# Kernel tuning notes

Hardware: AMD Instinct MI355X
Metric: run time of the kernel (lower is better)

Reference implementation:

```python
import jax, jax.numpy as jnp
import numpy as np

B = 1 << 20          # pixels (1024x1024 render)
RES = 512            # neural texture resolution
C_OFF = 8            # offset texture channels
C_RGB = 8            # rgb texture channels
HID = 32             # MLP hidden width
SLOPE = 0.01         # LeakyReLU negative slope (torch default)


def _leaky(x):
    return jnp.where(x >= 0, x, SLOPE * x)


def _mlp(x, params):
    # 3 hidden LeakyReLU layers + linear output, matching ThreeLayerMLP
    n = len(params)
    for i, (W, b) in enumerate(params):
        x = x @ W.T + b
        if i < n - 1:
            x = _leaky(x)
    return x


def _bilinear_wrap(tex, uv):
    # tex: (R, R, C) stored y-major; uv: (B, 2) in [0,1], wrapped (tiling texture)
    R = tex.shape[0]
    p = uv * R - 0.5
    i0 = jnp.floor(p).astype(jnp.int32)
    f = p - i0
    x0 = jnp.mod(i0[:, 0], R); x1 = jnp.mod(i0[:, 0] + 1, R)
    y0 = jnp.mod(i0[:, 1], R); y1 = jnp.mod(i0[:, 1] + 1, R)
    fx = f[:, 0:1]; fy = f[:, 1:2]
    v00 = tex[y0, x0]; v01 = tex[y0, x1]
    v10 = tex[y1, x0]; v11 = tex[y1, x1]
    return (v00 * (1 - fx) * (1 - fy) + v01 * fx * (1 - fy)
            + v10 * (1 - fx) * fy + v11 * fx * fy)


def _linear_params(key, n_in, n_out):
    W = jax.random.normal(key, (n_out, n_in), dtype=jnp.float32) * 0.01
    b = jnp.zeros((n_out,), dtype=jnp.float32)
    return W, b


def setup_inputs() -> dict:
    key = jax.random.key(0)
    ks = jax.random.split(key, 16)
    # directions: xy components of unit vectors, keep |xy| < 1
    camera_dir = (jax.random.uniform(ks[0], (B, 2), jnp.float32) - 0.5) * 1.2
    light_dir = (jax.random.uniform(ks[1], (B, 2), jnp.float32) - 0.5) * 1.2
    uv = jax.random.uniform(ks[2], (B, 2), jnp.float32)
    offset_tex = jax.random.normal(ks[3], (RES, RES, C_OFF), jnp.float32) * 0.1
    rgb_tex = jax.random.normal(ks[4], (RES, RES, C_RGB), jnp.float32) * 0.1
    # offset network: 10 -> 32 -> 32 -> 32 -> 1
    ow0, ob0 = _linear_params(ks[5], C_OFF + 2, HID)
    ow1, ob1 = _linear_params(ks[6], HID, HID)
    ow2, ob2 = _linear_params(ks[7], HID, HID)
    ow3, ob3 = _linear_params(ks[8], HID, 1)
    # rgb network: 12 -> 32 -> 32 -> 32 -> 3
    rw0, rb0 = _linear_params(ks[9], C_RGB + 4, HID)
    rw1, rb1 = _linear_params(ks[10], HID, HID)
    rw2, rb2 = _linear_params(ks[11], HID, HID)
    rw3, rb3 = _linear_params(ks[12], HID, 3)
    return dict(camera_dir=camera_dir, light_dir=light_dir, uv=uv,
                offset_tex=offset_tex, rgb_tex=rgb_tex,
                ow0=ow0, ob0=ob0, ow1=ow1, ob1=ob1, ow2=ow2, ob2=ob2, ow3=ow3, ob3=ob3,
                rw0=rw0, rb0=rb0, rw1=rw1, rb1=rb1, rw2=rw2, rb2=rb2, rw3=rw3, rb3=rb3)


def reference(camera_dir, light_dir, uv, offset_tex, rgb_tex,
              ow0, ob0, ow1, ob1, ow2, ob2, ow3, ob3,
              rw0, rb0, rw1, rb1, rw2, rb2, rw3, rb3):
    off_params = [(ow0, ob0), (ow1, ob1), (ow2, ob2), (ow3, ob3)]
    rgb_params = [(rw0, rb0), (rw1, rb1), (rw2, rb2), (rw3, rb3)]
    # offset branch: sample offset texture at uv, run tiny MLP -> neural depth
    off_lat = _bilinear_wrap(offset_tex, uv)                         # (B, 8)
    depth = _mlp(jnp.concatenate([off_lat, camera_dir], -1), off_params)  # (B, 1)
    # calculate_neural_offset: offset_uv = dir_xy / dir_z * depth
    z = jnp.sqrt(jnp.clip(1.0 - jnp.sum(camera_dir ** 2, -1, keepdims=True), 1e-6))
    uv2 = uv + camera_dir / z * depth                                # (B, 2)
    # rgb branch: sample rgb texture at offset intersection
    rgb_lat = _bilinear_wrap(rgb_tex, uv2)                           # (B, 8)
    rgb_in = jnp.concatenate([light_dir, camera_dir, rgb_lat], -1)   # (B, 12)
    return _mlp(rgb_in, rgb_params)                                  # (B, 3)
```

## Files before the change

kernel.cpp:

```cpp
#include <hip/hip_runtime.h>
#include <hip/hip_bf16.h>

static constexpr int BATCH = 1 << 20;
static constexpr size_t ILV_BYTES = (size_t)512 * 512 * 16 * 4;
static constexpr size_t WBLOB_BYTES = 768 * 16;

using f32x16 = __attribute__((ext_vector_type(16))) float;
using s16x8  = __attribute__((ext_vector_type(8))) short;
using u32x4  = __attribute__((ext_vector_type(4))) unsigned int;

__device__ __forceinline__ unsigned pkbf(float lo, float hi) {
  unsigned short a = __builtin_bit_cast(unsigned short, __float2bfloat16(lo));
  unsigned short b = __builtin_bit_cast(unsigned short, __float2bfloat16(hi));
  return (unsigned)a | ((unsigned)b << 16);
}

__device__ __forceinline__ u32x4 pack8(const float* __restrict__ p) {
  u32x4 r = {pkbf(p[0], p[1]), pkbf(p[2], p[3]), pkbf(p[4], p[5]), pkbf(p[6], p[7])};
  return r;
}

__device__ __forceinline__ f32x16 mfma_bf16(u32x4 a, u32x4 b, f32x16 c) {
  return __builtin_amdgcn_mfma_f32_32x32x16_bf16(
      __builtin_bit_cast(s16x8, a), __builtin_bit_cast(s16x8, b), c, 0, 0, 0);
}

__device__ __forceinline__ void act_pack_swap(f32x16 acc, u32x4& B0, u32x4& B1) {
  float r[16];
#pragma unroll
  for (int i = 0; i < 16; ++i) {
    float t = acc[i];
    r[i] = fmaxf(t, 0.01f * t);
  }
  unsigned pk[4][2];
#pragma unroll
  for (int b = 0; b < 4; ++b) {
    pk[b][0] = pkbf(r[4 * b + 0], r[4 * b + 1]);
    pk[b][1] = pkbf(r[4 * b + 2], r[4 * b + 3]);
  }
  auto r0 = __builtin_amdgcn_permlane32_swap(pk[0][0], pk[1][0], false, false);
  auto r1 = __builtin_amdgcn_permlane32_swap(pk[0][1], pk[1][1], false, false);
  auto r2 = __builtin_amdgcn_permlane32_swap(pk[2][0], pk[3][0], false, false);
  auto r3 = __builtin_amdgcn_permlane32_swap(pk[2][1], pk[3][1], false, false);
  B0[0] = r0[0]; B0[1] = r1[0]; B0[2] = r0[1]; B0[3] = r1[1];
  B1[0] = r2[0]; B1[1] = r3[0]; B1[2] = r2[1]; B1[3] = r3[1];
}

__device__ __forceinline__ f32x16 load_bias(const float* __restrict__ bp, int h) {
  f32x16 c;
#pragma unroll
  for (int b = 0; b < 4; ++b) {
    float4 t = *reinterpret_cast<const float4*>(bp + 8 * b + 4 * h);
    c[4 * b + 0] = t.x; c[4 * b + 1] = t.y; c[4 * b + 2] = t.z; c[4 * b + 3] = t.w;
  }
  return c;
}

template <bool ILV>
__device__ __forceinline__ float4 bilin4(const float* __restrict__ tex, float ux,
                                         float uy, int h, int which) {
  float px = ux * 512.0f - 0.5f;
  float py = uy * 512.0f - 0.5f;
  float fpx = floorf(px), fpy = floorf(py);
  float fx = px - fpx, fy = py - fpy;
  int ix = (int)fpx, iy = (int)fpy;
  int x0 = ix & 511, x1 = (ix + 1) & 511;
  int y0 = iy & 511, y1 = (iy + 1) & 511;
  constexpr int SH = ILV ? 4 : 3;
  const int co = (ILV ? (which << 3) : 0) + (h << 2);
  const float* p00 = tex + (((size_t)((y0 << 9) | x0) << SH) + co);
  const float* p01 = tex + (((size_t)((y0 << 9) | x1) << SH) + co);
  const float* p10 = tex + (((size_t)((y1 << 9) | x0) << SH) + co);
  const float* p11 = tex + (((size_t)((y1 << 9) | x1) << SH) + co);
  float4 a = *reinterpret_cast<const float4*>(p00);
  float4 b = *reinterpret_cast<const float4*>(p01);
  float4 c = *reinterpret_cast<const float4*>(p10);
  float4 d = *reinterpret_cast<const float4*>(p11);
  float gx = 1.0f - fx, gy = 1.0f - fy;
  float w00 = gx * gy, w01 = fx * gy, w10 = gx * fy, w11 = fx * fy;
  float4 o;
  o.x = fmaf(d.x, w11, fmaf(c.x, w10, fmaf(b.x, w01, a.x * w00)));
  o.y = fmaf(d.y, w11, fmaf(c.y, w10, fmaf(b.y, w01, a.y * w00)));
  o.z = fmaf(d.z, w11, fmaf(c.z, w10, fmaf(b.z, w01, a.z * w00)));
  o.w = fmaf(d.w, w11, fmaf(c.w, w10, fmaf(b.w, w01, a.w * w00)));
  return o;
}

__global__ void __launch_bounds__(256) tex_interleave(
    const float* __restrict__ t0, const float* __restrict__ t1,
    float* __restrict__ ws) {
  int i = blockIdx.x * 256 + threadIdx.x;
  int texel = i >> 2;
  int q = i & 3;
  const float* src = (q < 2 ? t0 : t1) + (((size_t)texel << 3) + ((q & 1) << 2));
  reinterpret_cast<float4*>(ws)[i] = *reinterpret_cast<const float4*>(src);
}

__global__ void __launch_bounds__(256) pack_weights(
    const float* __restrict__ ow0, const float* __restrict__ ow1,
    const float* __restrict__ ow2, const float* __restrict__ rw0,
    const float* __restrict__ rw1, const float* __restrict__ rw2,
    const float* __restrict__ rw3, u32x4* __restrict__ Wb) {
  int slot = blockIdx.x * 256 + threadIdx.x;
  if (slot < 768) {
    int F = slot % 12;
    int lb = slot / 12;
    int h = lb >> 5, m = lb & 31;
    u32x4 v = {0u, 0u, 0u, 0u};
    switch (F) {
      case 0:
        if (h == 0) v = pack8(ow0 + 10 * m);
        else { const float* p = ow0 + 10 * m + 8; v = u32x4{pkbf(p[0], p[1]), 0u, 0u, 0u}; }
        break;
      case 1: v = pack8(ow1 + 32 * m + 8 * h); break;
      case 2: v = pack8(ow1 + 32 * m + 16 + 8 * h); break;
      case 3: v = pack8(ow2 + 32 * m + 8 * h); break;
      case 4: v = pack8(ow2 + 32 * m + 16 + 8 * h); break;
      case 5:
        if (h == 0) v = pack8(rw0 + 12 * m);
        else { const float* p = rw0 + 12 * m + 8; v = u32x4{pkbf(p[0], p[1]), pkbf(p[2], p[3]), 0u, 0u}; }
        break;
      case 6: v = pack8(rw1 + 32 * m + 8 * h); break;
      case 7: v = pack8(rw1 + 32 * m + 16 + 8 * h); break;
      case 8: v = pack8(rw2 + 32 * m + 8 * h); break;
      case 9: v = pack8(rw2 + 32 * m + 16 + 8 * h); break;
      case 10: if (m < 3) v = pack8(rw3 + 32 * m + 8 * h); break;
      case 11: if (m < 3) v = pack8(rw3 + 32 * m + 16 + 8 * h); break;
    }
    Wb[slot] = v;
  }
}

template <bool ILV>
__global__ void __launch_bounds__(256) neumip_mfma(
    const float* __restrict__ cam_g, const float* __restrict__ light_g,
    const float* __restrict__ uv_g, const float* __restrict__ offset_tex,
    const float* __restrict__ rgb_tex, const float* __restrict__ wtex,
    const u32x4* __restrict__ Wb,
    const float* __restrict__ ow0, const float* __restrict__ ob0,
    const float* __restrict__ ow1, const float* __restrict__ ob1,
    const float* __restrict__ ow2, const float* __restrict__ ob2,
    const float* __restrict__ ow3, const float* __restrict__ ob3,
    const float* __restrict__ rw0, const float* __restrict__ rb0,
    const float* __restrict__ rw1, const float* __restrict__ rb1,
    const float* __restrict__ rw2, const float* __restrict__ rb2,
    const float* __restrict__ rw3, const float* __restrict__ rb3,
    float* __restrict__ out) {
  const int tid = threadIdx.x;
  const int lane = tid & 63;
  const int widx = tid >> 6;
  const int h = lane >> 5;
  const int sl = lane & 31;
  const int m = sl;
  const float* texO = ILV ? wtex : offset_tex;
  const float* texR = ILV ? wtex : rgb_tex;

  const int s1 = lane / 3, c1 = lane - 3 * s1;
  const int j2 = 64 + sl;
  const int s2 = j2 / 3, c2 = j2 - 3 * s2;

  const u32x4* Wl = Wb + (h * 32 + m) * 12;
  u32x4 A_o1, A_o2a, A_o2b, A_o3a, A_o3b, A_r1, A_r2a, A_r2b, A_r3a, A_r3b,
      A_r4a, A_r4b;
  if (ILV) {
    A_o1 = Wl[0];  A_o2a = Wl[1]; A_o2b = Wl[2]; A_o3a = Wl[3]; A_o3b = Wl[4];
    A_r1 = Wl[5];  A_r2a = Wl[6]; A_r2b = Wl[7]; A_r3a = Wl[8]; A_r3b = Wl[9];
    A_r4a = Wl[10]; A_r4b = Wl[11];
  } else {
    if (h == 0) {
      A_o1 = pack8(ow0 + 10 * m);
    } else {
      const float* p = ow0 + 10 * m + 8;
      A_o1 = u32x4{pkbf(p[0], p[1]), 0u, 0u, 0u};
    }
    A_o2a = pack8(ow1 + 32 * m + 8 * h);
    A_o2b = pack8(ow1 + 32 * m + 16 + 8 * h);
    A_o3a = pack8(ow2 + 32 * m + 8 * h);
    A_o3b = pack8(ow2 + 32 * m + 16 + 8 * h);
    if (h == 0) {
      A_r1 = pack8(rw0 + 12 * m);
    } else {
      const float* p = rw0 + 12 * m + 8;
      A_r1 = u32x4{pkbf(p[0], p[1]), pkbf(p[2], p[3]), 0u, 0u};
    }
    A_r2a = pack8(rw1 + 32 * m + 8 * h);
    A_r2b = pack8(rw1 + 32 * m + 16 + 8 * h);
    A_r3a = pack8(rw2 + 32 * m + 8 * h);
    A_r3b = pack8(rw2 + 32 * m + 16 + 8 * h);
    if (m < 3) {
      A_r4a = pack8(rw3 + 32 * m + 8 * h);
      A_r4b = pack8(rw3 + 32 * m + 16 + 8 * h);
    } else {
      A_r4a = u32x4{0u, 0u, 0u, 0u};
      A_r4b = u32x4{0u, 0u, 0u, 0u};
    }
  }

  f32x16 w3f;
#pragma unroll
  for (int b = 0; b < 4; ++b) {
    float4 t = *reinterpret_cast<const float4*>(ow3 + 8 * b + 4 * h);
    w3f[4 * b + 0] = t.x; w3f[4 * b + 1] = t.y;
    w3f[4 * b + 2] = t.z; w3f[4 * b + 3] = t.w;
  }
  const float b30 = rb3[0], b31 = rb3[1], b32 = rb3[2];
  const float ob3s = ob3[0];

  const float2* uv2g = reinterpret_cast<const float2*>(uv_g);
  const float2* cam2g = reinterpret_cast<const float2*>(cam_g);
  const float2* light2g = reinterpret_cast<const float2*>(light_g);

  const int NG = BATCH / 32;
  const int nw = (int)(gridDim.x * (blockDim.x >> 6));
  int g = (int)blockIdx.x * (int)(blockDim.x >> 6) + widx;
  if (g >= NG) return;

  float2 uvv = uv2g[g * 32 + sl];
  float2 cam = cam2g[g * 32 + sl];
  float2 light = light2g[g * 32 + sl];
  float4 ch = bilin4<ILV>(texO, uvv.x, uvv.y, h, 0);

#pragma unroll 1
  for (; g < NG; g += nw) {
    const int gn = (g + nw < NG) ? g + nw : g;
    const int Sn = gn * 32 + sl;
    float2 uvn = uv2g[Sn];
    float2 camn = cam2g[Sn];
    float2 lightn = light2g[Sn];

    unsigned V0 = pkbf(ch.x, ch.y), V1 = pkbf(ch.z, ch.w);
    auto t0 = __builtin_amdgcn_permlane32_swap(V0, V0, false, false);
    auto t1 = __builtin_amdgcn_permlane32_swap(V1, V1, false, false);
    unsigned camk = pkbf(cam.x, cam.y);
    u32x4 Bin;
    Bin[0] = h ? camk : V0;
    Bin[1] = h ? 0u : V1;
    Bin[2] = h ? 0u : t0[1];
    Bin[3] = h ? 0u : t1[1];

    f32x16 acc = load_bias(ob0, h);
    acc = mfma_bf16(A_o1, Bin, acc);
    u32x4 B0, B1;
    act_pack_swap(acc, B0, B1);
    acc = load_bias(ob1, h);
    acc = mfma_bf16(A_o2a, B0, acc);
    acc = mfma_bf16(A_o2b, B1, acc);
    act_pack_swap(acc, B0, B1);
    acc = load_bias(ob2, h);
    acc = mfma_bf16(A_o3a, B0, acc);
    acc = mfma_bf16(A_o3b, B1, acc);

    float part = 0.0f;
#pragma unroll
    for (int i = 0; i < 16; ++i) {
      float t = acc[i];
      t = fmaxf(t, 0.01f * t);
      part = fmaf(w3f[i], t, part);
    }
    float depth = part + __shfl_xor(part, 32) + ob3s;

    float s2f = fmaf(cam.x, cam.x, cam.y * cam.y);
    float z = sqrtf(fmaxf(1.0f - s2f, 1e-6f));
    float drz = depth * (1.0f / z);
    float u2x = fmaf(cam.x, drz, uvv.x);
    float u2y = fmaf(cam.y, drz, uvv.y);

    float4 chr = bilin4<ILV>(texR, u2x, u2y, h, 1);
    float4 chn = bilin4<ILV>(texO, uvn.x, uvn.y, h, 0);

    unsigned P0 = pkbf(chr.x, chr.y), P1 = pkbf(chr.z, chr.w);
    u32x4 Brin;
    Brin[0] = h ? P0 : pkbf(light.x, light.y);
    Brin[1] = h ? P1 : camk;
    Brin[2] = h ? 0u : P0;
    Brin[3] = h ? 0u : P1;

    acc = load_bias(rb0, h);
    acc = mfma_bf16(A_r1, Brin, acc);
    act_pack_swap(acc, B0, B1);
    acc = load_bias(rb1, h);
    acc = mfma_bf16(A_r2a, B0, acc);
    acc = mfma_bf16(A_r2b, B1, acc);
    act_pack_swap(acc, B0, B1);
    acc = load_bias(rb2, h);
    acc = mfma_bf16(A_r3a, B0, acc);
    acc = mfma_bf16(A_r3b, B1, acc);
    act_pack_swap(acc, B0, B1);
    f32x16 accf;
#pragma unroll
    for (int i = 0; i < 16; ++i) accf[i] = 0.0f;
    accf = mfma_bf16(A_r4a, B0, accf);
    accf = mfma_bf16(A_r4b, B1, accf);

    float o0 = accf[0] + b30, o1 = accf[1] + b31, o2 = accf[2] + b32;
    float a0 = __shfl(o0, s1), a1 = __shfl(o1, s1), a2 = __shfl(o2, s1);
    float v1 = (c1 == 0) ? a0 : ((c1 == 1) ? a1 : a2);
    float d0 = __shfl(o0, s2), d1 = __shfl(o1, s2), d2 = __shfl(o2, s2);
    float v2 = (c2 == 0) ? d0 : ((c2 == 1) ? d1 : d2);
    float* og = out + (size_t)g * 96;
    og[lane] = v1;
    if (h == 1) og[64 + sl] = v2;

    uvv = uvn; cam = camn; light = lightn; ch = chn;
  }
}

extern "C" void kernel_launch(void* const* d_in, const int* in_sizes, int n_in,
                              void* d_out, int out_size, void* d_ws, size_t ws_size,
                              hipStream_t stream) {
  const float* cam = (const float*)d_in[0];
  const float* light = (const float*)d_in[1];
  const float* uv = (const float*)d_in[2];
  const float* offset_tex = (const float*)d_in[3];
  const float* rgb_tex = (const float*)d_in[4];
  const float* ow0 = (const float*)d_in[5];
  const float* ob0 = (const float*)d_in[6];
  const float* ow1 = (const float*)d_in[7];
  const float* ob1 = (const float*)d_in[8];
  const float* ow2 = (const float*)d_in[9];
  const float* ob2 = (const float*)d_in[10];
  const float* ow3 = (const float*)d_in[11];
  const float* ob3 = (const float*)d_in[12];
  const float* rw0 = (const float*)d_in[13];
  const float* rb0 = (const float*)d_in[14];
  const float* rw1 = (const float*)d_in[15];
  const float* rb1 = (const float*)d_in[16];
  const float* rw2 = (const float*)d_in[17];
  const float* rb2 = (const float*)d_in[18];
  const float* rw3 = (const float*)d_in[19];
  const float* rb3 = (const float*)d_in[20];
  float* out = (float*)d_out;
  float* wtex = (float*)d_ws;
  u32x4* Wb = (u32x4*)((char*)d_ws + ILV_BYTES);

  dim3 block(256);
  if (ws_size >= ILV_BYTES + WBLOB_BYTES) {
    hipLaunchKernelGGL(tex_interleave, dim3(4096), block, 0, stream, offset_tex,
                       rgb_tex, wtex);
    hipLaunchKernelGGL(pack_weights, dim3(3), block, 0, stream, ow0, ow1, ow2,
                       rw0, rw1, rw2, rw3, Wb);
    hipLaunchKernelGGL(neumip_mfma<true>, dim3(2048), block, 0, stream, cam,
                       light, uv, offset_tex, rgb_tex, wtex, Wb, ow0, ob0, ow1,
                       ob1, ow2, ob2, ow3, ob3, rw0, rb0, rw1, rb1, rw2, rb2,
                       rw3, rb3, out);
  } else {
    hipLaunchKernelGGL(neumip_mfma<false>, dim3(2048), block, 0, stream, cam,
                       light, uv, offset_tex, rgb_tex, wtex, Wb, ow0, ob0, ow1,
                       ob1, ow2, ob2, ow3, ob3, rw0, rb0, rw1, rb1, rw2, rb2,
                       rw3, rb3, out);
  }
}
```

Baseline: 201.9 us.

## Interleave two 32-pixel groups per wave to overlap MFMA chains and gathers

```diff
diff --git a/kernel.cpp b/kernel.cpp
--- a/kernel.cpp
+++ b/kernel.cpp
@@ -210,98 +210,145 @@
   const float2* cam2g = reinterpret_cast<const float2*>(cam_g);
   const float2* light2g = reinterpret_cast<const float2*>(light_g);
 
-  const int NG = BATCH / 32;
+  const int NP = BATCH / 64;
   const int nw = (int)(gridDim.x * (blockDim.x >> 6));
-  int g = (int)blockIdx.x * (int)(blockDim.x >> 6) + widx;
-  if (g >= NG) return;
-
-  float2 uvv = uv2g[g * 32 + sl];
-  float2 cam = cam2g[g * 32 + sl];
-  float2 light = light2g[g * 32 + sl];
-  float4 ch = bilin4<ILV>(texO, uvv.x, uvv.y, h, 0);
+  int p = (int)blockIdx.x * (int)(blockDim.x >> 6) + widx;
 
 #pragma unroll 1
-  for (; g < NG; g += nw) {
-    const int gn = (g + nw < NG) ? g + nw : g;
-    const int Sn = gn * 32 + sl;
-    float2 uvn = uv2g[Sn];
-    float2 camn = cam2g[Sn];
-    float2 lightn = light2g[Sn];
-
-    unsigned V0 = pkbf(ch.x, ch.y), V1 = pkbf(ch.z, ch.w);
-    auto t0 = __builtin_amdgcn_permlane32_swap(V0, V0, false, false);
-    auto t1 = __builtin_amdgcn_permlane32_swap(V1, V1, false, false);
-    unsigned camk = pkbf(cam.x, cam.y);
-    u32x4 Bin;
-    Bin[0] = h ? camk : V0;
-    Bin[1] = h ? 0u : V1;
-    Bin[2] = h ? 0u : t0[1];
-    Bin[3] = h ? 0u : t1[1];
-
-    f32x16 acc = load_bias(ob0, h);
-    acc = mfma_bf16(A_o1, Bin, acc);
-    u32x4 B0, B1;
-    act_pack_swap(acc, B0, B1);
-    acc = load_bias(ob1, h);
-    acc = mfma_bf16(A_o2a, B0, acc);
-    acc = mfma_bf16(A_o2b, B1, acc);
-    act_pack_swap(acc, B0, B1);
-    acc = load_bias(ob2, h);
-    acc = mfma_bf16(A_o3a, B0, acc);
-    acc = mfma_bf16(A_o3b, B1, acc);
-
-    float part = 0.0f;
-#pragma unroll
-    for (int i = 0; i < 16; ++i) {
-      float t = acc[i];
-      t = fmaxf(t, 0.01f * t);
-      part = fmaf(w3f[i], t, part);
-    }
-    float depth = part + __shfl_xor(part, 32) + ob3s;
-
-    float s2f = fmaf(cam.x, cam.x, cam.y * cam.y);
-    float z = sqrtf(fmaxf(1.0f - s2f, 1e-6f));
-    float drz = depth * (1.0f / z);
-    float u2x = fmaf(cam.x, drz, uvv.x);
-    float u2y = fmaf(cam.y, drz, uvv.y);
-
-    float4 chr = bilin4<ILV>(texR, u2x, u2y, h, 1);
-    float4 chn = bilin4<ILV>(texO, uvn.x, uvn.y, h, 0);
-
-    unsigned P0 = pkbf(chr.x, chr.y), P1 = pkbf(chr.z, chr.w);
-    u32x4 Brin;
-    Brin[0] = h ? P0 : pkbf(light.x, light.y);
-    Brin[1] = h ? P1 : camk;
-    Brin[2] = h ? 0u : P0;
-    Brin[3] = h ? 0u : P1;
-
-    acc = load_bias(rb0, h);
-    acc = mfma_bf16(A_r1, Brin, acc);
-    act_pack_swap(acc, B0, B1);
-    acc = load_bias(rb1, h);
-    acc = mfma_bf16(A_r2a, B0, acc);
-    acc = mfma_bf16(A_r2b, B1, acc);
-    act_pack_swap(acc, B0, B1);
-    acc = load_bias(rb2, h);
-    acc = mfma_bf16(A_r3a, B0, acc);
-    acc = mfma_bf16(A_r3b, B1, acc);
-    act_pack_swap(acc, B0, B1);
-    f32x16 accf;
-#pragma unroll
-    for (int i = 0; i < 16; ++i) accf[i] = 0.0f;
-    accf = mfma_bf16(A_r4a, B0, accf);
-    accf = mfma_bf16(A_r4b, B1, accf);
-
-    float o0 = accf[0] + b30, o1 = accf[1] + b31, o2 = accf[2] + b32;
-    float a0 = __shfl(o0, s1), a1 = __shfl(o1, s1), a2 = __shfl(o2, s1);
-    float v1 = (c1 == 0) ? a0 : ((c1 == 1) ? a1 : a2);
-    float d0 = __shfl(o0, s2), d1 = __shfl(o1, s2), d2 = __shfl(o2, s2);
-    float v2 = (c2 == 0) ? d0 : ((c2 == 1) ? d1 : d2);
-    float* og = out + (size_t)g * 96;
-    og[lane] = v1;
-    if (h == 1) og[64 + sl] = v2;
-
-    uvv = uvn; cam = camn; light = lightn; ch = chn;
+  for (; p < NP; p += nw) {
+    const int gA = p << 1;
+
+    float2 uvv[2], cam[2], light[2];
+#pragma unroll
+    for (int u = 0; u < 2; ++u) {
+      const int S = (gA + u) * 32 + sl;
+      uvv[u] = uv2g[S];
+      cam[u] = cam2g[S];
+      light[u] = light2g[S];
+    }
+    float4 ch[2];
+#pragma unroll
+    for (int u = 0; u < 2; ++u)
+      ch[u] = bilin4<ILV>(texO, uvv[u].x, uvv[u].y, h, 0);
+
+    unsigned camk[2];
+    u32x4 Bin[2];
+#pragma unroll
+    for (int u = 0; u < 2; ++u) {
+      unsigned V0 = pkbf(ch[u].x, ch[u].y), V1 = pkbf(ch[u].z, ch[u].w);
+      auto t0 = __builtin_amdgcn_permlane32_swap(V0, V0, false, false);
+      auto t1 = __builtin_amdgcn_permlane32_swap(V1, V1, false, false);
+      camk[u] = pkbf(cam[u].x, cam[u].y);
+      Bin[u][0] = h ? camk[u] : V0;
+      Bin[u][1] = h ? 0u : V1;
+      Bin[u][2] = h ? 0u : t0[1];
+      Bin[u][3] = h ? 0u : t1[1];
+    }
+
+    f32x16 acc[2];
+    u32x4 B0[2], B1[2];
+    {
+      f32x16 cb = load_bias(ob0, h);
+#pragma unroll
+      for (int u = 0; u < 2; ++u) acc[u] = mfma_bf16(A_o1, Bin[u], cb);
+    }
+#pragma unroll
+    for (int u = 0; u < 2; ++u) act_pack_swap(acc[u], B0[u], B1[u]);
+    {
+      f32x16 cb = load_bias(ob1, h);
+#pragma unroll
+      for (int u = 0; u < 2; ++u) {
+        acc[u] = mfma_bf16(A_o2a, B0[u], cb);
+        acc[u] = mfma_bf16(A_o2b, B1[u], acc[u]);
+      }
+    }
+#pragma unroll
+    for (int u = 0; u < 2; ++u) act_pack_swap(acc[u], B0[u], B1[u]);
+    {
+      f32x16 cb = load_bias(ob2, h);
+#pragma unroll
+      for (int u = 0; u < 2; ++u) {
+        acc[u] = mfma_bf16(A_o3a, B0[u], cb);
+        acc[u] = mfma_bf16(A_o3b, B1[u], acc[u]);
+      }
+    }
+
+    float u2x[2], u2y[2];
+#pragma unroll
+    for (int u = 0; u < 2; ++u) {
+      float part = 0.0f;
+#pragma unroll
+      for (int i = 0; i < 16; ++i) {
+        float t = acc[u][i];
+        t = fmaxf(t, 0.01f * t);
+        part = fmaf(w3f[i], t, part);
+      }
+      float depth = part + __shfl_xor(part, 32) + ob3s;
+      float s2f = fmaf(cam[u].x, cam[u].x, cam[u].y * cam[u].y);
+      float z = sqrtf(fmaxf(1.0f - s2f, 1e-6f));
+      float drz = depth * (1.0f / z);
+      u2x[u] = fmaf(cam[u].x, drz, uvv[u].x);
+      u2y[u] = fmaf(cam[u].y, drz, uvv[u].y);
+    }
+
+    float4 chr[2];
+#pragma unroll
+    for (int u = 0; u < 2; ++u)
+      chr[u] = bilin4<ILV>(texR, u2x[u], u2y[u], h, 1);
+
+#pragma unroll
+    for (int u = 0; u < 2; ++u) {
+      unsigned P0 = pkbf(chr[u].x, chr[u].y), P1 = pkbf(chr[u].z, chr[u].w);
+      Bin[u][0] = h ? P0 : pkbf(light[u].x, light[u].y);
+      Bin[u][1] = h ? P1 : camk[u];
+      Bin[u][2] = h ? 0u : P0;
+      Bin[u][3] = h ? 0u : P1;
+    }
+
+    {
+      f32x16 cb = load_bias(rb0, h);
+#pragma unroll
+      for (int u = 0; u < 2; ++u) acc[u] = mfma_bf16(A_r1, Bin[u], cb);
+    }
+#pragma unroll
+    for (int u = 0; u < 2; ++u) act_pack_swap(acc[u], B0[u], B1[u]);
+    {
+      f32x16 cb = load_bias(rb1, h);
+#pragma unroll
+      for (int u = 0; u < 2; ++u) {
+        acc[u] = mfma_bf16(A_r2a, B0[u], cb);
+        acc[u] = mfma_bf16(A_r2b, B1[u], acc[u]);
+      }
+    }
+#pragma unroll
+    for (int u = 0; u < 2; ++u) act_pack_swap(acc[u], B0[u], B1[u]);
+    {
+      f32x16 cb = load_bias(rb2, h);
+#pragma unroll
+      for (int u = 0; u < 2; ++u) {
+        acc[u] = mfma_bf16(A_r3a, B0[u], cb);
+        acc[u] = mfma_bf16(A_r3b, B1[u], acc[u]);
+      }
+    }
+#pragma unroll
+    for (int u = 0; u < 2; ++u) act_pack_swap(acc[u], B0[u], B1[u]);
+
+#pragma unroll
+    for (int u = 0; u < 2; ++u) {
+      f32x16 accf;
+#pragma unroll
+      for (int i = 0; i < 16; ++i) accf[i] = 0.0f;
+      accf = mfma_bf16(A_r4a, B0[u], accf);
+      accf = mfma_bf16(A_r4b, B1[u], accf);
+      float o0 = accf[0] + b30, o1 = accf[1] + b31, o2 = accf[2] + b32;
+      float a0 = __shfl(o0, s1), a1 = __shfl(o1, s1), a2 = __shfl(o2, s1);
+      float v1 = (c1 == 0) ? a0 : ((c1 == 1) ? a1 : a2);
+      float d0 = __shfl(o0, s2), d1 = __shfl(o1, s2), d2 = __shfl(o2, s2);
+      float v2 = (c2 == 0) ? d0 : ((c2 == 1) ? d1 : d2);
+      float* og = out + (size_t)(gA + u) * 96;
+      og[lane] = v1;
+      if (h == 1) og[64 + sl] = v2;
+    }
   }
 }
 
```

Result: slower. 229.2 us (+13.5%).
